# Kernel optimization log

Hardware: AMD Instinct MI355X
Metric: run time of the kernel (lower is better)

Reference implementation:

```python
import jax, jax.numpy as jnp
import numpy as np
from jax import lax

# Production-scale RPN detection-head config
B, FH, FW, NA = 8, 200, 200, 9      # batch, fmap h, fmap w, anchors/cell
H, W = 800, 800                      # image dims
N = FH * FW * NA                     # 360k anchors per image
NMS_THR = 0.7
MIN_SIZE = 1e-3


def _make_anchors():
    scales = np.array([32.0, 64.0, 128.0])
    ratios = np.array([0.5, 1.0, 2.0])
    ws = (scales[:, None] * np.sqrt(1.0 / ratios)[None, :]).reshape(-1)  # [NA]
    hs = (scales[:, None] * np.sqrt(ratios)[None, :]).reshape(-1)
    sy, sx = H / FH, W / FW
    cx = (np.arange(FW) + 0.5) * sx
    cy = (np.arange(FH) + 0.5) * sy
    cxg, cyg = np.meshgrid(cx, cy)                     # [FH,FW]
    cxg = cxg[..., None]; cyg = cyg[..., None]         # [FH,FW,1]
    a = np.stack([cxg - ws / 2, cyg - hs / 2, cxg + ws / 2, cyg + hs / 2], axis=-1)
    return jnp.asarray(a.reshape(-1, 4), jnp.float32)  # [N,4] xyxy


def setup_inputs() -> dict:
    key = jax.random.key(0)
    k1, k2 = jax.random.split(key)
    cls_logits = jax.random.normal(k1, (B, N, 1), jnp.float32)
    reg_deltas = jax.random.normal(k2, (B, N, 4), jnp.float32) * 0.1  # sane exp(dw)
    anchors = jnp.broadcast_to(_make_anchors()[None], (B, N, 4))
    return {
        "cls_logits": cls_logits,
        "reg_deltas": reg_deltas,
        "anchors": anchors,
        "keep_pre_nms": 1000,
        "keep_post_nms": 300,
    }


def _offsets2boxes(deltas, anchors):
    aw = anchors[:, 2] - anchors[:, 0]
    ah = anchors[:, 3] - anchors[:, 1]
    acx = anchors[:, 0] + 0.5 * aw
    acy = anchors[:, 1] + 0.5 * ah
    cx = deltas[:, 0] * aw + acx
    cy = deltas[:, 1] * ah + acy
    w = jnp.exp(deltas[:, 2]) * aw
    h = jnp.exp(deltas[:, 3]) * ah
    return jnp.stack([cx - 0.5 * w, cy - 0.5 * h, cx + 0.5 * w, cy + 0.5 * h], axis=-1)


def _iou_matrix(b):
    area = (b[:, 2] - b[:, 0]) * (b[:, 3] - b[:, 1])
    lt = jnp.maximum(b[:, None, :2], b[None, :, :2])
    rb = jnp.minimum(b[:, None, 2:], b[None, :, 2:])
    wh = jnp.clip(rb - lt, 0.0)
    inter = wh[..., 0] * wh[..., 1]
    return inter / (area[:, None] + area[None, :] - inter + 1e-9)


def _detect_one(logit, delta, anc, pre, post):
    scores = jax.nn.sigmoid(logit.reshape(-1))             # [N]
    boxes = _offsets2boxes(delta.reshape(-1, 4), anc)      # [N,4]
    s, idx = lax.top_k(scores, pre)                        # sorted desc
    b = boxes[idx]                                         # [pre,4]
    # clip to image
    b = jnp.stack([
        jnp.clip(b[:, 0], 0.0, W), jnp.clip(b[:, 1], 0.0, H),
        jnp.clip(b[:, 2], 0.0, W), jnp.clip(b[:, 3], 0.0, H)], axis=-1)
    valid = ((b[:, 2] - b[:, 0]) >= MIN_SIZE) & ((b[:, 3] - b[:, 1]) >= MIN_SIZE)
    # greedy NMS on score-sorted boxes (mask-based, fixed shapes)
    iou = _iou_matrix(lax.stop_gradient(b))                # [pre,pre]
    j = jnp.arange(pre)

    def body(keep, i):
        sup = (iou[i] > NMS_THR) & (j > i) & keep[i]
        return keep & ~sup, None

    keep, _ = lax.scan(body, valid, jnp.arange(pre))
    # compact first `post` kept detections into fixed [post,5], zero-padded
    dets = jnp.concatenate([b, s[:, None]], axis=-1)       # [pre,5]
    rank = jnp.cumsum(keep) - 1
    tgt = jnp.where(keep & (rank < post), rank, post)
    out = jnp.zeros((post + 1, 5), dets.dtype).at[tgt].set(dets)[:post]
    return out


def reference(cls_logits, reg_deltas, anchors, keep_pre_nms, keep_post_nms):
    f = lambda l, d, a: _detect_one(l, d, a, keep_pre_nms, keep_post_nms)
    return jax.vmap(f)(cls_logits, reg_deltas, anchors)    # [B,post,5]
```

## Files before the change

### kernel.cpp

```cpp
#include <hip/hip_runtime.h>
#include <stdint.h>
#include <math.h>

typedef unsigned long long u64;
typedef unsigned int u32;

#define NPI   360000
#define B_IMG 8
#define PRE   1000
#define POST  300
#define CAP   4096
#define NMSF  0.7f
#define IMG_W 800.0f
#define IMG_H 800.0f

#define NBIN    4096
#define KSHIFT  20
#define NGRP    64
#define CHUNK_C 48
#define F4PB_C  (NPI / 4 / CHUNK_C)
#define EPB_C   (NPI / CHUNK_C)
#define PBLK    128

#define THR_LOGIT 2.62f

#define VALID_OFF   256
#define BCNT_OFF    4096
#define PCAND_OFF   8192
#define BOX_OFF     401408
#define SCORE_OFF   529408
#define MASK_OFF    561408

#define LDSROWS 496
#define NMS_T   320
#define RBLK    16

__device__ __forceinline__ u32 fkey(float f) {
  u32 u = __float_as_uint(f);
  return (u & 0x80000000u) ? ~u : (u | 0x80000000u);
}
__device__ __forceinline__ u64 rl64(u64 v, int lane) {
  u32 lo = (u32)__builtin_amdgcn_readlane((int)(u32)v, lane);
  u32 hi = (u32)__builtin_amdgcn_readlane((int)(u32)(v >> 32), lane);
  return ((u64)hi << 32) | lo;
}
__device__ __forceinline__ u64 sx64(u64 v, int m) {
  u32 lo = (u32)__shfl_xor((int)(u32)v, m, 64);
  u32 hi = (u32)__shfl_xor((int)(u32)(v >> 32), m, 64);
  return ((u64)hi << 32) | lo;
}

__global__ __launch_bounds__(256) void k_compact(const float* __restrict__ logits,
                                                 u32* __restrict__ bcnt_blk,
                                                 u64* __restrict__ pcand,
                                                 u64* __restrict__ validw) {
  __shared__ u32 bcnt;
  const int img = blockIdx.y, c = blockIdx.x;
  const int t = threadIdx.x;
  const u32 FK0 = fkey(THR_LOGIT);
  if (t == 0) bcnt = 0;
  if (c == 0 && t < 16) validw[img * 16 + t] = 0;
  __syncthreads();
  const float4* L = (const float4*)(logits + (size_t)img * NPI) + (size_t)c * F4PB_C;
  u64* P = pcand + ((size_t)img * CHUNK_C + c) * PBLK;
  const int ebase = c * EPB_C;
#pragma unroll
  for (int k = 0; k < 8; k++) {
    int i = t + k * 256;
    if (i < F4PB_C) {
      float4 v = L[i];
      float xs[4] = {v.x, v.y, v.z, v.w};
#pragma unroll
      for (int q = 0; q < 4; q++) {
        float x = xs[q];
        if (fkey(x) >= FK0) {
          float ef = (float)exp(-(double)x);
          float sg = 1.0f / (1.0f + ef);
          u32 e = (u32)(ebase + 4 * i + q);
          u32 p = atomicAdd(&bcnt, 1u);
          if (p < PBLK)
            P[p] = ((u64)fkey(sg) << 32) | (u64)(0xFFFFFFFFu - e);
        }
      }
    }
  }
  __syncthreads();
  if (t == 0) bcnt_blk[img * CHUNK_C + c] = bcnt;
}

__device__ __forceinline__ void emit_row(
    int img, int row, u64 key,
    const float* __restrict__ deltas, const float* __restrict__ anchors,
    float4* __restrict__ boxes, float* __restrict__ scores, u64* __restrict__ validw) {
  u32 hi  = (u32)(key >> 32);
  u32 idx = 0xFFFFFFFFu - (u32)(key & 0xFFFFFFFFu);
  u32 su  = (hi & 0x80000000u) ? (hi ^ 0x80000000u) : ~hi;
  float sc = __uint_as_float(su);
  size_t off = (size_t)img * NPI + idx;
  float4 d = ((const float4*)deltas)[off];
  float4 a = ((const float4*)anchors)[off];
  float aw = a.z - a.x, ah = a.w - a.y;
  float acx = a.x + 0.5f * aw, acy = a.y + 0.5f * ah;
  float cx = d.x * aw + acx, cy = d.y * ah + acy;
  float w = expf(d.z) * aw, h = expf(d.w) * ah;
  float x1 = cx - 0.5f * w, y1 = cy - 0.5f * h;
  float x2 = cx + 0.5f * w, y2 = cy + 0.5f * h;
  x1 = fminf(fmaxf(x1, 0.f), IMG_W);
  y1 = fminf(fmaxf(y1, 0.f), IMG_H);
  x2 = fminf(fmaxf(x2, 0.f), IMG_W);
  y2 = fminf(fmaxf(y2, 0.f), IMG_H);
  boxes[img * PRE + row]  = make_float4(x1, y1, x2, y2);
  scores[img * PRE + row] = sc;
  if (((x2 - x1) >= 1e-3f) && ((y2 - y1) >= 1e-3f))
    atomicOr(&validw[img * 16 + (row >> 6)], 1ull << (row & 63));
}

__global__ __launch_bounds__(256) void k_rank(
    const float* __restrict__ logits,
    const float* __restrict__ deltas, const float* __restrict__ anchors,
    const u32* __restrict__ bcnt_blk, const u64* __restrict__ pcand,
    float4* __restrict__ boxes, float* __restrict__ scores, u64* __restrict__ validw) {
  __shared__ u64 skey[CAP];
  __shared__ u32 pc[4][256];
  __shared__ u32 scnt[CHUNK_C], soff[CHUNK_C];
  __shared__ int sn, sbad, stb;
  __shared__ u32 rc;
  const int img = blockIdx.y;
  const int tid = threadIdx.x;
  const int w = tid >> 6, l = tid & 63;
  if (tid < CHUNK_C) scnt[tid] = bcnt_blk[img * CHUNK_C + tid];
  if (tid == 0) { sbad = 0; stb = 0; rc = 0; }
  __syncthreads();
  if (tid < 64) {
    u32 m = (tid < CHUNK_C) ? (scnt[tid] > (u32)PBLK ? (u32)PBLK : scnt[tid]) : 0u;
    u64 bb = __ballot(tid < CHUNK_C && scnt[tid] > (u32)PBLK);
    u32 x = m;
#pragma unroll
    for (int off = 1; off < 64; off <<= 1) {
      u32 o = (u32)__shfl_up((int)x, off, 64);
      if (l >= off) x += o;
    }
    if (tid < CHUNK_C) soff[tid] = x - m;
    u32 tot = (u32)__builtin_amdgcn_readlane((int)x, 63);
    if (tid == 0) {
      sn = (int)tot;
      if (bb != 0ull || tot < (u32)PRE || tot > (u32)CAP) sbad = 1;
    }
  }
  __syncthreads();
  int n = sn;
  const int base = blockIdx.x * 256;
  if (!sbad) {
    if (base >= n) return;
    for (int c = w; c < CHUNK_C; c += 4) {
      u32 mc = scnt[c];
      u32 off = soff[c];
      const u64* src = pcand + ((size_t)img * CHUNK_C + c) * PBLK;
      for (u32 j = l; j < mc; j += 64) skey[off + j] = src[j];
    }
    __syncthreads();
  } else {
    u32* hh = (u32*)skey;
    for (int i = tid; i < NBIN; i += 256) hh[i] = 0;
    __syncthreads();
    const float4* L = (const float4*)(logits + (size_t)img * NPI);
    for (int i = tid; i < NPI / 4; i += 256) {
      float4 v = L[i];
      atomicAdd(&hh[fkey(v.x) >> KSHIFT], 1u);
      atomicAdd(&hh[fkey(v.y) >> KSHIFT], 1u);
      atomicAdd(&hh[fkey(v.z) >> KSHIFT], 1u);
      atomicAdd(&hh[fkey(v.w) >> KSHIFT], 1u);
    }
    __syncthreads();
    if (tid < 64) {
      u32 cg = 0;
      for (int b = 0; b < NBIN / NGRP; b++) cg += hh[tid * (NBIN / NGRP) + b];
      u32 suf = cg;
#pragma unroll
      for (int off = 1; off < 64; off <<= 1) {
        u32 o = (u32)__shfl_down((int)suf, off, 64);
        if (tid + off < 64) suf += o;
      }
      u32 sx = suf - cg;
      u64 bal = __ballot(suf >= (u32)PRE && sx < (u32)PRE);
      if (bal) {
        int gc = __builtin_ctzll(bal);
        u32 s_above = (u32)__shfl((int)sx, gc, 64);
        u32 fb = hh[gc * (NBIN / NGRP) + tid];
        u32 fsuf = fb;
#pragma unroll
        for (int off = 1; off < 64; off <<= 1) {
          u32 o = (u32)__shfl_down((int)fsuf, off, 64);
          if (tid + off < 64) fsuf += o;
        }
        u32 fincl = fsuf + s_above, fexcl = fincl - fb;
        if (fincl >= (u32)PRE && fexcl < (u32)PRE) stb = gc * (NBIN / NGRP) + tid;
      }
    }
    __syncthreads();
    const int tb = stb;
    for (int i = tid; i < NPI / 4; i += 256) {
      float4 v = L[i];
      float xs[4] = {v.x, v.y, v.z, v.w};
#pragma unroll
      for (int q = 0; q < 4; q++) {
        float x = xs[q];
        if ((int)(fkey(x) >> KSHIFT) >= tb) {
          float ef = (float)exp(-(double)x);
          float sg = 1.0f / (1.0f + ef);
          u32 e = (u32)(4 * i + q);
          u32 p = atomicAdd(&rc, 1u);
          if (p < CAP) skey[p] = ((u64)fkey(sg) << 32) | (u64)(0xFFFFFFFFu - e);
        }
      }
    }
    __syncthreads();
    n = (int)(rc < (u32)CAP ? rc : (u32)CAP);
    for (int r = tid; r < n; r += 256) {
      u64 kr = skey[r];
      int cr = 0;
      for (int j = 0; j < n; j++) cr += (skey[j] > kr);
      if (cr < PRE) emit_row(img, cr, kr, deltas, anchors, boxes, scores, validw);
    }
    return;
  }
  const int r0 = base + l, r1 = r0 + 64, r2 = r0 + 128, r3 = r0 + 192;
  u64 k0 = (r0 < n) ? skey[r0] : 0ull;
  u64 k1 = (r1 < n) ? skey[r1] : 0ull;
  u64 k2 = (r2 < n) ? skey[r2] : 0ull;
  u64 k3 = (r3 < n) ? skey[r3] : 0ull;
  int c0 = 0, c1 = 0, c2 = 0, c3 = 0;
  const int js = (w * n) >> 2, je = ((w + 1) * n) >> 2;
  int j = js;
  for (; j + 8 <= je; j += 8) {
    u64 b0 = skey[j + 0], b1 = skey[j + 1], b2 = skey[j + 2], b3 = skey[j + 3];
    u64 b4 = skey[j + 4], b5 = skey[j + 5], b6 = skey[j + 6], b7 = skey[j + 7];
    c0 += (b0 > k0) + (b1 > k0) + (b2 > k0) + (b3 > k0)
        + (b4 > k0) + (b5 > k0) + (b6 > k0) + (b7 > k0);
    c1 += (b0 > k1) + (b1 > k1) + (b2 > k1) + (b3 > k1)
        + (b4 > k1) + (b5 > k1) + (b6 > k1) + (b7 > k1);
    c2 += (b0 > k2) + (b1 > k2) + (b2 > k2) + (b3 > k2)
        + (b4 > k2) + (b5 > k2) + (b6 > k2) + (b7 > k2);
    c3 += (b0 > k3) + (b1 > k3) + (b2 > k3) + (b3 > k3)
        + (b4 > k3) + (b5 > k3) + (b6 > k3) + (b7 > k3);
  }
  for (; j < je; j++) {
    u64 kj = skey[j];
    c0 += (kj > k0); c1 += (kj > k1); c2 += (kj > k2); c3 += (kj > k3);
  }
  pc[w][l]       = (u32)c0;
  pc[w][l + 64]  = (u32)c1;
  pc[w][l + 128] = (u32)c2;
  pc[w][l + 192] = (u32)c3;
  __syncthreads();
  const int rr = base + tid;
  if (rr < n) {
    int c = (int)(pc[0][tid] + pc[1][tid] + pc[2][tid] + pc[3][tid]);
    if (c < PRE) emit_row(img, c, skey[rr], deltas, anchors, boxes, scores, validw);
  }
}

__global__ __launch_bounds__(512) void k_iou(const float4* __restrict__ boxes,
                                             u64* __restrict__ mask) {
  __shared__ float4 sb[1024];
  __shared__ float  sa[1024];
  const int img = blockIdx.y, rb = blockIdx.x;
  const int tid = threadIdx.x;
  for (int j = tid; j < 1024; j += 512) {
    float4 b = (j < PRE) ? boxes[img * PRE + j] : make_float4(0.f, 0.f, 0.f, 0.f);
    sb[j] = b;
    sa[j] = (b.z - b.x) * (b.w - b.y);
  }
  __syncthreads();
  const int i  = rb * 32 + (tid & 31);
  const int wv = tid >> 5;
  const bool rowok = (i < PRE);
  const int cbase = wv << 6;
  if (cbase + 63 < rb * 32) {
    if (rowok) mask[((size_t)img * PRE + i) * 16 + wv] = 0ull;
    return;
  }
  const float4 bi = sb[i];
  const float  ai = sa[i];
  u64 bits = 0;
#pragma unroll
  for (int k = 0; k < 64; k++) {
    int c = cbase + k;
    float4 bc = sb[c];
    float ac  = sa[c];
    float ltx = fmaxf(bi.x, bc.x), lty = fmaxf(bi.y, bc.y);
    float rbx = fminf(bi.z, bc.z), rby = fminf(bi.w, bc.w);
    float iw = fmaxf(rbx - ltx, 0.f), ih = fmaxf(rby - lty, 0.f);
    float inter = iw * ih;
    float iou = inter / (ai + ac - inter + 1e-9f);
    bits |= (iou > NMSF) ? (1ull << k) : 0ull;
  }
  int d = i - cbase;
  u64 gtmask = (d < 0) ? ~0ull : ((d >= 63) ? 0ull : (~0ull << (d + 1)));
  int rem = PRE - cbase;
  u64 tmask = (rem >= 64) ? ~0ull : ((rem <= 0) ? 0ull : ((1ull << rem) - 1ull));
  bits &= gtmask & tmask;
  if (rowok) mask[((size_t)img * PRE + i) * 16 + wv] = bits;
}

__global__ __launch_bounds__(NMS_T) void k_nms(
    const u64* __restrict__ mask, const u64* __restrict__ validw,
    const float4* __restrict__ boxes, const float* __restrict__ scores,
    float* __restrict__ out) {
  __shared__ u64 smask[LDSROWS * 16];
  __shared__ int skeeplist[POST];
  __shared__ int skept;
  const int img = blockIdx.x;
  const int tid = threadIdx.x;
  const u64* M = mask + (size_t)img * PRE * 16;
  u64 diag[16];
  if (tid < 64) {
#pragma unroll
    for (int cc = 0; cc < 16; cc++) {
      int row = cc * 64 + tid;
      diag[cc] = (row < PRE) ? M[(size_t)row * 16 + cc] : 0ull;
    }
  }
  for (int e = tid; e < LDSROWS * 16; e += NMS_T) smask[e] = M[e];
  __syncthreads();
  if (tid < 64) {
    const int lane = tid;
    const int w = lane & 15, g = lane >> 4;
    u64 rem = ~0ull;
    if (lane < 16) {
      rem = ~validw[img * 16 + lane];
      if (lane == 15) rem |= 0xFFFFFF0000000000ull;
    }
    int kept = 0;
#pragma unroll
    for (int cc = 0; cc < 16; cc++) {
      u64 alive = ~rl64(rem, cc);
      int kept0 = kept;
      while (alive != 0ull && kept < POST) {
        int r = __builtin_ctzll(alive);
        if (lane == 0) skeeplist[kept] = cc * 64 + r;
        kept++;
        u64 sup = rl64(diag[cc], r);
        alive &= ~sup;
        alive &= ~(1ull << r);
      }
      int nc = kept - kept0;
      if (nc > 0 && kept < POST && cc < 15) {
        u64 part = 0;
        for (int j = g; j < nc; j += 4) {
          int row = skeeplist[kept0 + j];
          part |= (row < LDSROWS) ? smask[row * 16 + w] : M[(size_t)row * 16 + w];
        }
        part |= sx64(part, 16);
        part |= sx64(part, 32);
        rem |= part;
      }
      if (kept >= POST) break;
    }
    if (lane == 0) skept = kept;
  }
  __syncthreads();
  if (tid < POST) {
    float4 bx = make_float4(0.f, 0.f, 0.f, 0.f);
    float  sc = 0.f;
    if (tid < skept) {
      int i = skeeplist[tid];
      bx = boxes[img * PRE + i];
      sc = scores[img * PRE + i];
    }
    float* o = out + ((size_t)img * POST + tid) * 5;
    o[0] = bx.x; o[1] = bx.y; o[2] = bx.z; o[3] = bx.w; o[4] = sc;
  }
}

extern "C" void kernel_launch(void* const* d_in, const int* in_sizes, int n_in,
                              void* d_out, int out_size, void* d_ws, size_t ws_size,
                              hipStream_t stream) {
  const float* logits  = (const float*)d_in[0];
  const float* deltas  = (const float*)d_in[1];
  const float* anchors = (const float*)d_in[2];
  float* out = (float*)d_out;
  char* ws = (char*)d_ws;

  u64* validw   = (u64*)(ws + VALID_OFF);
  u32* bcnt_blk = (u32*)(ws + BCNT_OFF);
  u64* pcand    = (u64*)(ws + PCAND_OFF);
  float4* boxes = (float4*)(ws + BOX_OFF);
  float* scores = (float*)(ws + SCORE_OFF);
  u64* mask     = (u64*)(ws + MASK_OFF);

  dim3 gc(CHUNK_C, B_IMG);
  k_compact<<<gc, 256, 0, stream>>>(logits, bcnt_blk, pcand, validw);
  dim3 gr(RBLK, B_IMG);
  k_rank<<<gr, 256, 0, stream>>>(logits, deltas, anchors, bcnt_blk, pcand,
                                 boxes, scores, validw);
  dim3 g2(32, B_IMG);
  k_iou<<<g2, 512, 0, stream>>>(boxes, mask);
  k_nms<<<B_IMG, NMS_T, 0, stream>>>(mask, validw, boxes, scores, out);
}
```

Before: 183.1 us.

## Fuse compact+rank and iou+nms kernels using atomic ticket counters

Merges the four-kernel pipeline into two. The last RANKB blocks of the compaction grid spin-wait for all chunks of their image and then do the rank/emit step. The IoU blocks use a last-block-done counter so the final block per image runs the greedy NMS. This removes two kernel launches and their gaps, at the cost of spin-waiting blocks, a memset for the counters, and reliance on all 48 blocks per image being co-resident.

```diff
diff --git a/kernel.cpp b/kernel.cpp
--- a/kernel.cpp
+++ b/kernel.cpp
@@ -21,10 +21,14 @@
 #define F4PB_C  (NPI / 4 / CHUNK_C)
 #define EPB_C   (NPI / CHUNK_C)
 #define PBLK    128
+#define RANKB   7
 
 #define THR_LOGIT 2.62f
 
+#define C1_OFF      0
+#define C2_OFF      64
 #define VALID_OFF   256
+#define ZERO_BYTES  1280
 #define BCNT_OFF    4096
 #define PCAND_OFF   8192
 #define BOX_OFF     401408
@@ -32,8 +36,6 @@
 #define MASK_OFF    561408
 
 #define LDSROWS 496
-#define NMS_T   320
-#define RBLK    16
 
 __device__ __forceinline__ u32 fkey(float f) {
   u32 u = __float_as_uint(f);
@@ -48,44 +50,6 @@
   u32 lo = (u32)__shfl_xor((int)(u32)v, m, 64);
   u32 hi = (u32)__shfl_xor((int)(u32)(v >> 32), m, 64);
   return ((u64)hi << 32) | lo;
-}
-
-__global__ __launch_bounds__(256) void k_compact(const float* __restrict__ logits,
-                                                 u32* __restrict__ bcnt_blk,
-                                                 u64* __restrict__ pcand,
-                                                 u64* __restrict__ validw) {
-  __shared__ u32 bcnt;
-  const int img = blockIdx.y, c = blockIdx.x;
-  const int t = threadIdx.x;
-  const u32 FK0 = fkey(THR_LOGIT);
-  if (t == 0) bcnt = 0;
-  if (c == 0 && t < 16) validw[img * 16 + t] = 0;
-  __syncthreads();
-  const float4* L = (const float4*)(logits + (size_t)img * NPI) + (size_t)c * F4PB_C;
-  u64* P = pcand + ((size_t)img * CHUNK_C + c) * PBLK;
-  const int ebase = c * EPB_C;
-#pragma unroll
-  for (int k = 0; k < 8; k++) {
-    int i = t + k * 256;
-    if (i < F4PB_C) {
-      float4 v = L[i];
-      float xs[4] = {v.x, v.y, v.z, v.w};
-#pragma unroll
-      for (int q = 0; q < 4; q++) {
-        float x = xs[q];
-        if (fkey(x) >= FK0) {
-          float ef = (float)exp(-(double)x);
-          float sg = 1.0f / (1.0f + ef);
-          u32 e = (u32)(ebase + 4 * i + q);
-          u32 p = atomicAdd(&bcnt, 1u);
-          if (p < PBLK)
-            P[p] = ((u64)fkey(sg) << 32) | (u64)(0xFFFFFFFFu - e);
-        }
-      }
-    }
-  }
-  __syncthreads();
-  if (t == 0) bcnt_blk[img * CHUNK_C + c] = bcnt;
 }
 
 __device__ __forceinline__ void emit_row(
@@ -115,18 +79,61 @@
     atomicOr(&validw[img * 16 + (row >> 6)], 1ull << (row & 63));
 }
 
-__global__ __launch_bounds__(256) void k_rank(
+__global__ __launch_bounds__(256) void k_compact_rank(
     const float* __restrict__ logits,
     const float* __restrict__ deltas, const float* __restrict__ anchors,
-    const u32* __restrict__ bcnt_blk, const u64* __restrict__ pcand,
-    float4* __restrict__ boxes, float* __restrict__ scores, u64* __restrict__ validw) {
+    u32* __restrict__ bcnt_blk, u64* __restrict__ pcand,
+    float4* __restrict__ boxes, float* __restrict__ scores,
+    u64* __restrict__ validw, u32* __restrict__ c1) {
   __shared__ u64 skey[CAP];
   __shared__ u32 pc[4][256];
   __shared__ u32 scnt[CHUNK_C], soff[CHUNK_C];
-  __shared__ int sn, sbad, stb;
-  __shared__ u32 rc;
-  const int img = blockIdx.y;
+  __shared__ int sn, sbad, stb, sticket;
+  __shared__ u32 rc, bcnt;
+  const int img = blockIdx.y, c = blockIdx.x;
   const int tid = threadIdx.x;
+  const u32 FK0 = fkey(THR_LOGIT);
+  if (tid == 0) bcnt = 0;
+  __syncthreads();
+  {
+    const float4* L = (const float4*)(logits + (size_t)img * NPI) + (size_t)c * F4PB_C;
+    u64* P = pcand + ((size_t)img * CHUNK_C + c) * PBLK;
+    const int ebase = c * EPB_C;
+#pragma unroll
+    for (int k = 0; k < 8; k++) {
+      int i = tid + k * 256;
+      if (i < F4PB_C) {
+        float4 v = L[i];
+        float xs[4] = {v.x, v.y, v.z, v.w};
+#pragma unroll
+        for (int q = 0; q < 4; q++) {
+          float x = xs[q];
+          if (fkey(x) >= FK0) {
+            float ef = (float)exp(-(double)x);
+            float sg = 1.0f / (1.0f + ef);
+            u32 e = (u32)(ebase + 4 * i + q);
+            u32 p = atomicAdd(&bcnt, 1u);
+            if (p < PBLK)
+              P[p] = ((u64)fkey(sg) << 32) | (u64)(0xFFFFFFFFu - e);
+          }
+        }
+      }
+    }
+    __syncthreads();
+    if (tid == 0) bcnt_blk[img * CHUNK_C + c] = bcnt;
+  }
+  __threadfence();
+  if (tid == 0) sticket = (int)atomicAdd(&c1[img], 1u);
+  __syncthreads();
+  const int rk = sticket - (CHUNK_C - RANKB);
+  if (rk < 0) return;
+  if (tid == 0) {
+    while (__hip_atomic_load(&c1[img], __ATOMIC_ACQUIRE, __HIP_MEMORY_SCOPE_AGENT)
+           < (u32)CHUNK_C)
+      __builtin_amdgcn_s_sleep(8);
+  }
+  __syncthreads();
+  __threadfence();
   const int w = tid >> 6, l = tid & 63;
   if (tid < CHUNK_C) scnt[tid] = bcnt_blk[img * CHUNK_C + tid];
   if (tid == 0) { sbad = 0; stb = 0; rc = 0; }
@@ -149,16 +156,53 @@
   }
   __syncthreads();
   int n = sn;
-  const int base = blockIdx.x * 256;
   if (!sbad) {
-    if (base >= n) return;
-    for (int c = w; c < CHUNK_C; c += 4) {
-      u32 mc = scnt[c];
-      u32 off = soff[c];
-      const u64* src = pcand + ((size_t)img * CHUNK_C + c) * PBLK;
+    if (rk * 256 >= n) return;
+    for (int cc = w; cc < CHUNK_C; cc += 4) {
+      u32 mc = scnt[cc];
+      u32 off = soff[cc];
+      const u64* src = pcand + ((size_t)img * CHUNK_C + cc) * PBLK;
       for (u32 j = l; j < mc; j += 64) skey[off + j] = src[j];
     }
     __syncthreads();
+    for (int win = rk; win * 256 < n; win += RANKB) {
+      const int base = win * 256;
+      const int r0 = base + l, r1 = r0 + 64, r2 = r0 + 128, r3 = r0 + 192;
+      u64 k0 = (r0 < n) ? skey[r0] : 0ull;
+      u64 k1 = (r1 < n) ? skey[r1] : 0ull;
+      u64 k2 = (r2 < n) ? skey[r2] : 0ull;
+      u64 k3 = (r3 < n) ? skey[r3] : 0ull;
+      int c0 = 0, c1v = 0, c2v = 0, c3v = 0;
+      const int js = (w * n) >> 2, je = ((w + 1) * n) >> 2;
+      int j = js;
+      for (; j + 8 <= je; j += 8) {
+        u64 b0 = skey[j + 0], b1 = skey[j + 1], b2 = skey[j + 2], b3 = skey[j + 3];
+        u64 b4 = skey[j + 4], b5 = skey[j + 5], b6 = skey[j + 6], b7 = skey[j + 7];
+        c0  += (b0 > k0) + (b1 > k0) + (b2 > k0) + (b3 > k0)
+             + (b4 > k0) + (b5 > k0) + (b6 > k0) + (b7 > k0);
+        c1v += (b0 > k1) + (b1 > k1) + (b2 > k1) + (b3 > k1)
+             + (b4 > k1) + (b5 > k1) + (b6 > k1) + (b7 > k1);
+        c2v += (b0 > k2) + (b1 > k2) + (b2 > k2) + (b3 > k2)
+             + (b4 > k2) + (b5 > k2) + (b6 > k2) + (b7 > k2);
+        c3v += (b0 > k3) + (b1 > k3) + (b2 > k3) + (b3 > k3)
+             + (b4 > k3) + (b5 > k3) + (b6 > k3) + (b7 > k3);
+      }
+      for (; j < je; j++) {
+        u64 kj = skey[j];
+        c0 += (kj > k0); c1v += (kj > k1); c2v += (kj > k2); c3v += (kj > k3);
+      }
+      pc[w][l]       = (u32)c0;
+      pc[w][l + 64]  = (u32)c1v;
+      pc[w][l + 128] = (u32)c2v;
+      pc[w][l + 192] = (u32)c3v;
+      __syncthreads();
+      const int rr = base + tid;
+      if (rr < n) {
+        int cr = (int)(pc[0][tid] + pc[1][tid] + pc[2][tid] + pc[3][tid]);
+        if (cr < PRE) emit_row(img, cr, skey[rr], deltas, anchors, boxes, scores, validw);
+      }
+      __syncthreads();
+    }
   } else {
     u32* hh = (u32*)skey;
     for (int i = tid; i < NBIN; i += 256) hh[i] = 0;
@@ -222,96 +266,60 @@
       for (int j = 0; j < n; j++) cr += (skey[j] > kr);
       if (cr < PRE) emit_row(img, cr, kr, deltas, anchors, boxes, scores, validw);
     }
-    return;
-  }
-  const int r0 = base + l, r1 = r0 + 64, r2 = r0 + 128, r3 = r0 + 192;
-  u64 k0 = (r0 < n) ? skey[r0] : 0ull;
-  u64 k1 = (r1 < n) ? skey[r1] : 0ull;
-  u64 k2 = (r2 < n) ? skey[r2] : 0ull;
-  u64 k3 = (r3 < n) ? skey[r3] : 0ull;
-  int c0 = 0, c1 = 0, c2 = 0, c3 = 0;
-  const int js = (w * n) >> 2, je = ((w + 1) * n) >> 2;
-  int j = js;
-  for (; j + 8 <= je; j += 8) {
-    u64 b0 = skey[j + 0], b1 = skey[j + 1], b2 = skey[j + 2], b3 = skey[j + 3];
-    u64 b4 = skey[j + 4], b5 = skey[j + 5], b6 = skey[j + 6], b7 = skey[j + 7];
-    c0 += (b0 > k0) + (b1 > k0) + (b2 > k0) + (b3 > k0)
-        + (b4 > k0) + (b5 > k0) + (b6 > k0) + (b7 > k0);
-    c1 += (b0 > k1) + (b1 > k1) + (b2 > k1) + (b3 > k1)
-        + (b4 > k1) + (b5 > k1) + (b6 > k1) + (b7 > k1);
-    c2 += (b0 > k2) + (b1 > k2) + (b2 > k2) + (b3 > k2)
-        + (b4 > k2) + (b5 > k2) + (b6 > k2) + (b7 > k2);
-    c3 += (b0 > k3) + (b1 > k3) + (b2 > k3) + (b3 > k3)
-        + (b4 > k3) + (b5 > k3) + (b6 > k3) + (b7 > k3);
-  }
-  for (; j < je; j++) {
-    u64 kj = skey[j];
-    c0 += (kj > k0); c1 += (kj > k1); c2 += (kj > k2); c3 += (kj > k3);
-  }
-  pc[w][l]       = (u32)c0;
-  pc[w][l + 64]  = (u32)c1;
-  pc[w][l + 128] = (u32)c2;
-  pc[w][l + 192] = (u32)c3;
-  __syncthreads();
-  const int rr = base + tid;
-  if (rr < n) {
-    int c = (int)(pc[0][tid] + pc[1][tid] + pc[2][tid] + pc[3][tid]);
-    if (c < PRE) emit_row(img, c, skey[rr], deltas, anchors, boxes, scores, validw);
-  }
-}
-
-__global__ __launch_bounds__(512) void k_iou(const float4* __restrict__ boxes,
-                                             u64* __restrict__ mask) {
-  __shared__ float4 sb[1024];
-  __shared__ float  sa[1024];
+  }
+}
+
+__global__ __launch_bounds__(512) void k_iou_nms(
+    const float4* __restrict__ boxes, const float* __restrict__ scores,
+    const u64* __restrict__ validw, u64* __restrict__ mask,
+    float* __restrict__ out, u32* __restrict__ c2) {
+  __shared__ union {
+    struct { float4 sb[1024]; float sa[1024]; } iou;
+    struct { u64 smask[LDSROWS * 16]; int keeplist[POST]; int kept; } nms;
+  } lds;
+  __shared__ int slast;
   const int img = blockIdx.y, rb = blockIdx.x;
   const int tid = threadIdx.x;
   for (int j = tid; j < 1024; j += 512) {
     float4 b = (j < PRE) ? boxes[img * PRE + j] : make_float4(0.f, 0.f, 0.f, 0.f);
-    sb[j] = b;
-    sa[j] = (b.z - b.x) * (b.w - b.y);
-  }
-  __syncthreads();
-  const int i  = rb * 32 + (tid & 31);
-  const int wv = tid >> 5;
-  const bool rowok = (i < PRE);
-  const int cbase = wv << 6;
-  if (cbase + 63 < rb * 32) {
-    if (rowok) mask[((size_t)img * PRE + i) * 16 + wv] = 0ull;
-    return;
-  }
-  const float4 bi = sb[i];
-  const float  ai = sa[i];
-  u64 bits = 0;
-#pragma unroll
-  for (int k = 0; k < 64; k++) {
-    int c = cbase + k;
-    float4 bc = sb[c];
-    float ac  = sa[c];
-    float ltx = fmaxf(bi.x, bc.x), lty = fmaxf(bi.y, bc.y);
-    float rbx = fminf(bi.z, bc.z), rby = fminf(bi.w, bc.w);
-    float iw = fmaxf(rbx - ltx, 0.f), ih = fmaxf(rby - lty, 0.f);
-    float inter = iw * ih;
-    float iou = inter / (ai + ac - inter + 1e-9f);
-    bits |= (iou > NMSF) ? (1ull << k) : 0ull;
-  }
-  int d = i - cbase;
-  u64 gtmask = (d < 0) ? ~0ull : ((d >= 63) ? 0ull : (~0ull << (d + 1)));
-  int rem = PRE - cbase;
-  u64 tmask = (rem >= 64) ? ~0ull : ((rem <= 0) ? 0ull : ((1ull << rem) - 1ull));
-  bits &= gtmask & tmask;
-  if (rowok) mask[((size_t)img * PRE + i) * 16 + wv] = bits;
-}
-
-__global__ __launch_bounds__(NMS_T) void k_nms(
-    const u64* __restrict__ mask, const u64* __restrict__ validw,
-    const float4* __restrict__ boxes, const float* __restrict__ scores,
-    float* __restrict__ out) {
-  __shared__ u64 smask[LDSROWS * 16];
-  __shared__ int skeeplist[POST];
-  __shared__ int skept;
-  const int img = blockIdx.x;
-  const int tid = threadIdx.x;
+    lds.iou.sb[j] = b;
+    lds.iou.sa[j] = (b.z - b.x) * (b.w - b.y);
+  }
+  __syncthreads();
+  {
+    const int i  = rb * 32 + (tid & 31);
+    const int wv = tid >> 5;
+    const bool rowok = (i < PRE);
+    const int cbase = wv << 6;
+    u64 bits = 0;
+    if (cbase + 63 >= rb * 32) {
+      const float4 bi = lds.iou.sb[i];
+      const float  ai = lds.iou.sa[i];
+#pragma unroll
+      for (int k = 0; k < 64; k++) {
+        int cc = cbase + k;
+        float4 bc = lds.iou.sb[cc];
+        float ac  = lds.iou.sa[cc];
+        float ltx = fmaxf(bi.x, bc.x), lty = fmaxf(bi.y, bc.y);
+        float rbx = fminf(bi.z, bc.z), rby = fminf(bi.w, bc.w);
+        float iw = fmaxf(rbx - ltx, 0.f), ih = fmaxf(rby - lty, 0.f);
+        float inter = iw * ih;
+        float iou = inter / (ai + ac - inter + 1e-9f);
+        bits |= (iou > NMSF) ? (1ull << k) : 0ull;
+      }
+      int d = i - cbase;
+      u64 gtmask = (d < 0) ? ~0ull : ((d >= 63) ? 0ull : (~0ull << (d + 1)));
+      int rem = PRE - cbase;
+      u64 tmask = (rem >= 64) ? ~0ull : ((rem <= 0) ? 0ull : ((1ull << rem) - 1ull));
+      bits &= gtmask & tmask;
+    }
+    if (rowok) mask[((size_t)img * PRE + i) * 16 + wv] = bits;
+  }
+  __threadfence();
+  if (tid == 0) slast = ((int)atomicAdd(&c2[img], 1u) == 31);
+  __syncthreads();
+  if (!slast) return;
+  __threadfence();
   const u64* M = mask + (size_t)img * PRE * 16;
   u64 diag[16];
   if (tid < 64) {
@@ -321,7 +329,7 @@
       diag[cc] = (row < PRE) ? M[(size_t)row * 16 + cc] : 0ull;
     }
   }
-  for (int e = tid; e < LDSROWS * 16; e += NMS_T) smask[e] = M[e];
+  for (int e = tid; e < LDSROWS * 16; e += 512) lds.nms.smask[e] = M[e];
   __syncthreads();
   if (tid < 64) {
     const int lane = tid;
@@ -338,7 +346,7 @@
       int kept0 = kept;
       while (alive != 0ull && kept < POST) {
         int r = __builtin_ctzll(alive);
-        if (lane == 0) skeeplist[kept] = cc * 64 + r;
+        if (lane == 0) lds.nms.keeplist[kept] = cc * 64 + r;
         kept++;
         u64 sup = rl64(diag[cc], r);
         alive &= ~sup;
@@ -348,8 +356,9 @@
       if (nc > 0 && kept < POST && cc < 15) {
         u64 part = 0;
         for (int j = g; j < nc; j += 4) {
-          int row = skeeplist[kept0 + j];
-          part |= (row < LDSROWS) ? smask[row * 16 + w] : M[(size_t)row * 16 + w];
+          int row = lds.nms.keeplist[kept0 + j];
+          part |= (row < LDSROWS) ? lds.nms.smask[row * 16 + w]
+                                  : M[(size_t)row * 16 + w];
         }
         part |= sx64(part, 16);
         part |= sx64(part, 32);
@@ -357,19 +366,19 @@
       }
       if (kept >= POST) break;
     }
-    if (lane == 0) skept = kept;
-  }
-  __syncthreads();
-  if (tid < POST) {
+    if (lane == 0) lds.nms.kept = kept;
+  }
+  __syncthreads();
+  for (int o = tid; o < POST; o += 512) {
     float4 bx = make_float4(0.f, 0.f, 0.f, 0.f);
     float  sc = 0.f;
-    if (tid < skept) {
-      int i = skeeplist[tid];
-      bx = boxes[img * PRE + i];
-      sc = scores[img * PRE + i];
-    }
-    float* o = out + ((size_t)img * POST + tid) * 5;
-    o[0] = bx.x; o[1] = bx.y; o[2] = bx.z; o[3] = bx.w; o[4] = sc;
+    if (o < lds.nms.kept) {
+      int i2 = lds.nms.keeplist[o];
+      bx = boxes[img * PRE + i2];
+      sc = scores[img * PRE + i2];
+    }
+    float* op = out + ((size_t)img * POST + o) * 5;
+    op[0] = bx.x; op[1] = bx.y; op[2] = bx.z; op[3] = bx.w; op[4] = sc;
   }
 }
 
@@ -382,6 +391,8 @@
   float* out = (float*)d_out;
   char* ws = (char*)d_ws;
 
+  u32* c1       = (u32*)(ws + C1_OFF);
+  u32* c2       = (u32*)(ws + C2_OFF);
   u64* validw   = (u64*)(ws + VALID_OFF);
   u32* bcnt_blk = (u32*)(ws + BCNT_OFF);
   u64* pcand    = (u64*)(ws + PCAND_OFF);
@@ -389,12 +400,10 @@
   float* scores = (float*)(ws + SCORE_OFF);
   u64* mask     = (u64*)(ws + MASK_OFF);
 
+  hipMemsetAsync(ws, 0, ZERO_BYTES, stream);
   dim3 gc(CHUNK_C, B_IMG);
-  k_compact<<<gc, 256, 0, stream>>>(logits, bcnt_blk, pcand, validw);
-  dim3 gr(RBLK, B_IMG);
-  k_rank<<<gr, 256, 0, stream>>>(logits, deltas, anchors, bcnt_blk, pcand,
-                                 boxes, scores, validw);
+  k_compact_rank<<<gc, 256, 0, stream>>>(logits, deltas, anchors, bcnt_blk, pcand,
+                                         boxes, scores, validw, c1);
   dim3 g2(32, B_IMG);
-  k_iou<<<g2, 512, 0, stream>>>(boxes, mask);
-  k_nms<<<B_IMG, NMS_T, 0, stream>>>(mask, validw, boxes, scores, out);
-}
+  k_iou_nms<<<g2, 512, 0, stream>>>(boxes, scores, validw, mask, out, c2);
+}
```

Measured after the change: 278.4 us. 52.1% more time.
